# Kernel tuning notes

Measured on AMD Instinct MI355X. Metric: run time of the kernel, lower is better.

## Reference

```python
import jax, jax.numpy as jnp
import numpy as np

N, T, D, P, NB = 32768, 128, 32, 16, 15


def setup_inputs() -> dict:
    key = jax.random.key(0)
    ks = jax.random.split(key, 8)
    S = jax.random.normal(ks[0], (N, T, 1), dtype=jnp.float32)
    L_dyn = jax.random.normal(ks[1], (N, T, D), dtype=jnp.float32)
    C_static = jax.random.normal(ks[2], (N, P), dtype=jnp.float32)
    Y = jax.random.randint(ks[3], (N, T, 1), 0, 2).astype(jnp.float32)
    mask = jnp.ones((N, T), dtype=jnp.float32)
    return {
        "S": S, "L_dyn": L_dyn, "C_static": C_static, "Y": Y, "mask": mask,
        "psi": jnp.array([0.5], jnp.float32),
        "gamma_A": jnp.array([0.1], jnp.float32),
        "w_gamma_dyn": 0.05 * jax.random.normal(ks[4], (D,), dtype=jnp.float32),
        "w_gamma_static": 0.05 * jax.random.normal(ks[5], (P,), dtype=jnp.float32),
        "log_sigma_Z": jnp.array([-0.5], jnp.float32),
        "beta_0": jnp.array([-4.0], jnp.float32),
        "beta_Z": jnp.array([0.3], jnp.float32),
        "beta_bins": jnp.zeros((NB,), jnp.float32),
        "w_beta_dyn": 0.1 * jax.random.normal(ks[6], (D,), dtype=jnp.float32),
        "w_beta_static": 0.1 * jax.random.normal(ks[7], (P,), dtype=jnp.float32),
        "beta_time": jnp.array([0.03], jnp.float32),
    }


def reference(S, L_dyn, C_static, Y, mask, psi, gamma_A, w_gamma_dyn,
              w_gamma_static, log_sigma_Z, beta_0, beta_Z, beta_bins,
              w_beta_dyn, w_beta_static, beta_time):
    n, t_len = S.shape[0], S.shape[1]
    nb = beta_bins.shape[0]
    edges = jnp.linspace(-2.5, 2.5, nb + 1).astype(S.dtype)
    # torch.bucketize(s, edges[1:-1]) (right=False) == searchsorted side='left'
    idx = jnp.clip(jnp.searchsorted(edges[1:-1], S[..., 0], side='left'), 0, nb - 1)
    bin_eff = beta_bins[idx][..., None]            # (N,T,1) == (A_bin * beta_bins).sum(-1)
    sigma_sq = jnp.exp(log_sigma_Z)[0] ** 2        # sigma_Z^2
    gd = L_dyn @ w_gamma_dyn[:, None]              # (N,T,1) gamma_dyn(L)
    bd = L_dyn @ w_beta_dyn[:, None]               # (N,T,1) beta_dyn(L)
    gs = (C_static @ w_gamma_static)[:, None]      # (N,1) gamma_static(C)
    bs = (C_static @ w_beta_static)[:, None]       # (N,1) beta_static(C)
    tt = jnp.arange(t_len, dtype=S.dtype) / 30.0   # beta_time * (t/30)

    xs = (
        jnp.swapaxes(S, 0, 1),        # (T,N,1)
        jnp.swapaxes(gd, 0, 1),
        jnp.swapaxes(bd, 0, 1),
        jnp.swapaxes(bin_eff, 0, 1),
        jnp.swapaxes(Y, 0, 1),
        mask.T[:, :, None],           # (T,N,1)
        tt,
    )
    psi_s, gA, bZ, b0, bT = psi[0], gamma_A[0], beta_Z[0], beta_0[0], beta_time[0]

    def step(carry, x):
        Z_mean, Z_var, ll = carry
        A_t, gd_t, bd_t, be_t, Y_t, m_t, t_s = x
        # latent transition prior
        Z_pred_mean = psi_s * Z_mean + gA * A_t + gd_t + gs
        Z_pred_var = psi_s ** 2 * Z_var + sigma_sq
        # outcome probability
        logit = b0 + bZ * Z_pred_mean + be_t + bd_t + bs + bT * t_s
        prob = jax.nn.sigmoid(jnp.clip(logit, -20.0, 20.0))
        # approximate Kalman (Laplace) update from Y
        grad = (Y_t - prob) * bZ * m_t
        hess = bZ ** 2 * prob * (1.0 - prob) * m_t + 1e-6
        Z_post_var = 1.0 / (1.0 / (Z_pred_var + 1e-8) + hess)
        Z_post_mean = Z_pred_mean + Z_post_var * grad
        ll_t = ((Y_t * jnp.log(prob + 1e-10)
                 + (1.0 - Y_t) * jnp.log(1.0 - prob + 1e-10)) * m_t).sum()
        return (Z_post_mean, Z_post_var, ll + ll_t), (Z_post_mean, Z_post_var)

    init = (jnp.zeros((n, 1), S.dtype), jnp.ones((n, 1), S.dtype),
            jnp.zeros((), S.dtype))
    (_, _, ll), (Zf, Zv) = jax.lax.scan(step, init, xs)
    return jnp.swapaxes(Zf, 0, 1), jnp.swapaxes(Zv, 0, 1), ll
```

## Files before the change

kernel.cpp:

```cpp
#include <hip/hip_runtime.h>

#define T_LEN 128
#define NB_BINS 15

__global__ __launch_bounds__(256) void k_fused(
    const float4* __restrict__ S4,
    const float4* __restrict__ Y4,
    const float4* __restrict__ M4,
    const float4* __restrict__ C4,
    const float4* __restrict__ L4,
    const float4* __restrict__ wgd4,
    const float4* __restrict__ wbd4,
    const float4* __restrict__ wgs4,
    const float4* __restrict__ wbs4,
    const float*  __restrict__ p_psi,
    const float*  __restrict__ p_gA,
    const float*  __restrict__ p_lsz,
    const float*  __restrict__ p_b0,
    const float*  __restrict__ p_bZ,
    const float*  __restrict__ p_bbins,
    const float*  __restrict__ p_bT,
    float* __restrict__ zf,
    float* __restrict__ zv,
    float* __restrict__ ll_out)
{
    __shared__ float sbins[NB_BINS];
    if (threadIdx.x < NB_BINS) sbins[threadIdx.x] = p_bbins[threadIdx.x];
    __syncthreads();

    const int gtid = blockIdx.x * blockDim.x + threadIdx.x;
    const int n = gtid >> 2;
    const int s = gtid & 3;

    const float4 wga = wgd4[s * 2],     wgb = wgd4[s * 2 + 1];
    const float4 wba = wbd4[s * 2],     wbb = wbd4[s * 2 + 1];

    const float psi  = p_psi[0];
    const float gA   = p_gA[0];
    const float e    = expf(p_lsz[0]);
    const float sig2 = e * e;
    const float b0   = p_b0[0];
    const float bZ   = p_bZ[0];
    const float bT   = p_bT[0];
    const float psi2 = psi * psi;
    const float bZ2  = bZ * bZ;

    float gs, bs;
    {
        const float4 c  = C4[n * 4 + s];
        const float4 wg = wgs4[s];
        const float4 wb = wbs4[s];
        gs = c.x * wg.x + c.y * wg.y + c.z * wg.z + c.w * wg.w;
        bs = c.x * wb.x + c.y * wb.y + c.z * wb.z + c.w * wb.w;
        gs += __shfl_xor(gs, 1, 64); gs += __shfl_xor(gs, 2, 64);
        bs += __shfl_xor(bs, 1, 64); bs += __shfl_xor(bs, 2, 64);
    }

    const size_t lb  = (size_t)n * T_LEN * 8 + (size_t)s * 2;
    const int    sbi = n * (T_LEN / 4);

    float4 Lc0 = L4[lb + 0*8], Lc1 = L4[lb + 0*8 + 1];
    float4 Lc2 = L4[lb + 1*8], Lc3 = L4[lb + 1*8 + 1];
    float4 Lc4 = L4[lb + 2*8], Lc5 = L4[lb + 2*8 + 1];
    float4 Lc6 = L4[lb + 3*8], Lc7 = L4[lb + 3*8 + 1];
    float4 sc = S4[sbi], yc = Y4[sbi], mc = M4[sbi];

    float zm = 0.0f, zvv = 1.0f, ll = 0.0f;

#define STEP(J, LA, LB, SS, YY, MM, PMOUT, PVOUT) do {                        \
        const float s_v = (SS), y_v = (YY), m_v = (MM);                       \
        float g   = LA.x*wga.x + LA.y*wga.y + LA.z*wga.z + LA.w*wga.w         \
                  + LB.x*wgb.x + LB.y*wgb.y + LB.z*wgb.z + LB.w*wgb.w;        \
        float bdv = LA.x*wba.x + LA.y*wba.y + LA.z*wba.z + LA.w*wba.w         \
                  + LB.x*wbb.x + LB.y*wbb.y + LB.z*wbb.z + LB.w*wbb.w;        \
        g   += __shfl_xor(g,   1, 64); g   += __shfl_xor(g,   2, 64);         \
        bdv += __shfl_xor(bdv, 1, 64); bdv += __shfl_xor(bdv, 2, 64);         \
        int cnt = (int)fmaxf(0.0f, fminf(14.0f,                               \
                      ceilf(fmaf(s_v, 3.0f, 7.5f)) - 1.0f));                  \
        const float be    = sbins[cnt];                                       \
        const float zpm   = psi * zm + gA * s_v + g + gs;                     \
        const float zpv   = psi2 * zvv + sig2;                                \
        float logit = b0 + bZ * zpm + be + bdv + bs                           \
                    + bT * ((float)(4 * k + (J)) / 30.0f);                    \
        logit = fminf(fmaxf(logit, -20.0f), 20.0f);                           \
        const float prob  = 1.0f / (1.0f + expf(-logit));                     \
        const float grad  = (y_v - prob) * bZ * m_v;                          \
        const float hess  = bZ2 * prob * (1.0f - prob) * m_v + 1e-6f;         \
        const float pvv   = 1.0f / (1.0f / (zpv + 1e-8f) + hess);             \
        const float pmm   = zpm + pvv * grad;                                 \
        ll += (y_v * logf(prob + 1e-10f)                                      \
             + (1.0f - y_v) * logf(1.0f - prob + 1e-10f)) * m_v;              \
        zm = pmm; zvv = pvv; PMOUT = pmm; PVOUT = pvv;                        \
    } while (0)

    for (int k = 0; k < T_LEN / 4; ++k) {
        const int kn = (k + 1 < T_LEN / 4) ? (k + 1) : k;
        const size_t lbn = lb + (size_t)(4 * kn) * 8;
        float4 Ln0 = L4[lbn + 0*8], Ln1 = L4[lbn + 0*8 + 1];
        float4 Ln2 = L4[lbn + 1*8], Ln3 = L4[lbn + 1*8 + 1];
        float4 Ln4 = L4[lbn + 2*8], Ln5 = L4[lbn + 2*8 + 1];
        float4 Ln6 = L4[lbn + 3*8], Ln7 = L4[lbn + 3*8 + 1];
        float4 snn = S4[sbi + kn], ynn = Y4[sbi + kn], mnn = M4[sbi + kn];

        float pm0, pm1, pm2, pm3, pv0, pv1, pv2, pv3;
        STEP(0, Lc0, Lc1, sc.x, yc.x, mc.x, pm0, pv0);
        STEP(1, Lc2, Lc3, sc.y, yc.y, mc.y, pm1, pv1);
        STEP(2, Lc4, Lc5, sc.z, yc.z, mc.z, pm2, pv2);
        STEP(3, Lc6, Lc7, sc.w, yc.w, mc.w, pm3, pv3);

        const float pmsel = (s == 0) ? pm0 : (s == 1) ? pm1 : (s == 2) ? pm2 : pm3;
        const float pvsel = (s == 0) ? pv0 : (s == 1) ? pv1 : (s == 2) ? pv2 : pv3;
        const size_t oidx = (size_t)n * T_LEN + 4 * k + s;
        zf[oidx] = pmsel;
        zv[oidx] = pvsel;

        Lc0 = Ln0; Lc1 = Ln1; Lc2 = Ln2; Lc3 = Ln3;
        Lc4 = Ln4; Lc5 = Ln5; Lc6 = Ln6; Lc7 = Ln7;
        sc = snn; yc = ynn; mc = mnn;
    }
#undef STEP

    float lv = (s == 0) ? ll : 0.0f;
    #pragma unroll
    for (int off = 1; off < 64; off <<= 1) lv += __shfl_xor(lv, off, 64);
    if ((threadIdx.x & 63) == 0) atomicAdd(ll_out, lv);
}

extern "C" void kernel_launch(void* const* d_in, const int* in_sizes, int n_in,
                              void* d_out, int out_size, void* d_ws, size_t ws_size,
                              hipStream_t stream) {
    const float* S     = (const float*)d_in[0];
    const float* L     = (const float*)d_in[1];
    const float* C     = (const float*)d_in[2];
    const float* Y     = (const float*)d_in[3];
    const float* M     = (const float*)d_in[4];
    const float* psi   = (const float*)d_in[5];
    const float* gA    = (const float*)d_in[6];
    const float* wgd   = (const float*)d_in[7];
    const float* wgs   = (const float*)d_in[8];
    const float* lsz   = (const float*)d_in[9];
    const float* b0    = (const float*)d_in[10];
    const float* bZ    = (const float*)d_in[11];
    const float* bbins = (const float*)d_in[12];
    const float* wbd   = (const float*)d_in[13];
    const float* wbs   = (const float*)d_in[14];
    const float* bT    = (const float*)d_in[15];

    const int NT    = in_sizes[0];
    const int n_seq = NT / T_LEN;

    float* zf = (float*)d_out;
    float* zv = zf + NT;
    float* ll = zf + 2 * (size_t)NT;

    hipMemsetAsync((void*)ll, 0, sizeof(float), stream);

    const int threads = 256;
    const int blocks  = (n_seq * 4) / threads;
    k_fused<<<blocks, threads, 0, stream>>>(
        reinterpret_cast<const float4*>(S),
        reinterpret_cast<const float4*>(Y),
        reinterpret_cast<const float4*>(M),
        reinterpret_cast<const float4*>(C),
        reinterpret_cast<const float4*>(L),
        reinterpret_cast<const float4*>(wgd),
        reinterpret_cast<const float4*>(wbd),
        reinterpret_cast<const float4*>(wgs),
        reinterpret_cast<const float4*>(wbs),
        psi, gA, lsz, b0, bZ, bbins, bT,
        zf, zv, ll);
}
```

Before: 177.8 us.

## Distribute log-likelihood across lanes, interleave L loads, use fast intrinsics

Each of the four lanes sharing a sequence now computes the log-likelihood term only for its own timestep, instead of all four lanes redundantly evaluating two logs per step. The L_dyn loads are remapped so adjacent lanes read adjacent float4s, and the dyn-weight slices are permuted to match. Exact exp, log and divisions are replaced with __expf, __logf and hardware reciprocal intrinsics, and the 1/30 time scale is folded into one constant. This trims redundant transcendental work and improves load coalescing, at the cost of slightly lower numerical precision.

```diff
diff --git a/kernel.cpp b/kernel.cpp
--- a/kernel.cpp
+++ b/kernel.cpp
@@ -32,16 +32,16 @@
     const int n = gtid >> 2;
     const int s = gtid & 3;
 
-    const float4 wga = wgd4[s * 2],     wgb = wgd4[s * 2 + 1];
-    const float4 wba = wbd4[s * 2],     wbb = wbd4[s * 2 + 1];
+    const float4 wga = wgd4[s],     wgb = wgd4[s + 4];
+    const float4 wba = wbd4[s],     wbb = wbd4[s + 4];
 
     const float psi  = p_psi[0];
     const float gA   = p_gA[0];
-    const float e    = expf(p_lsz[0]);
+    const float e    = __expf(p_lsz[0]);
     const float sig2 = e * e;
     const float b0   = p_b0[0];
     const float bZ   = p_bZ[0];
-    const float bT   = p_bT[0];
+    const float bT30 = p_bT[0] * (1.0f / 30.0f);
     const float psi2 = psi * psi;
     const float bZ2  = bZ * bZ;
 
@@ -56,18 +56,18 @@
         bs += __shfl_xor(bs, 1, 64); bs += __shfl_xor(bs, 2, 64);
     }
 
-    const size_t lb  = (size_t)n * T_LEN * 8 + (size_t)s * 2;
+    const size_t lb  = (size_t)n * T_LEN * 8;
     const int    sbi = n * (T_LEN / 4);
 
-    float4 Lc0 = L4[lb + 0*8], Lc1 = L4[lb + 0*8 + 1];
-    float4 Lc2 = L4[lb + 1*8], Lc3 = L4[lb + 1*8 + 1];
-    float4 Lc4 = L4[lb + 2*8], Lc5 = L4[lb + 2*8 + 1];
-    float4 Lc6 = L4[lb + 3*8], Lc7 = L4[lb + 3*8 + 1];
+    float4 Lc0 = L4[lb + 0*8 + s], Lc1 = L4[lb + 0*8 + 4 + s];
+    float4 Lc2 = L4[lb + 1*8 + s], Lc3 = L4[lb + 1*8 + 4 + s];
+    float4 Lc4 = L4[lb + 2*8 + s], Lc5 = L4[lb + 2*8 + 4 + s];
+    float4 Lc6 = L4[lb + 3*8 + s], Lc7 = L4[lb + 3*8 + 4 + s];
     float4 sc = S4[sbi], yc = Y4[sbi], mc = M4[sbi];
 
     float zm = 0.0f, zvv = 1.0f, ll = 0.0f;
 
-#define STEP(J, LA, LB, SS, YY, MM, PMOUT, PVOUT) do {                        \
+#define STEP(J, LA, LB, SS, YY, MM, PMOUT, PVOUT, PROBOUT) do {               \
         const float s_v = (SS), y_v = (YY), m_v = (MM);                       \
         float g   = LA.x*wga.x + LA.y*wga.y + LA.z*wga.z + LA.w*wga.w         \
                   + LB.x*wgb.x + LB.y*wgb.y + LB.z*wgb.z + LB.w*wgb.w;        \
@@ -81,32 +81,31 @@
         const float zpm   = psi * zm + gA * s_v + g + gs;                     \
         const float zpv   = psi2 * zvv + sig2;                                \
         float logit = b0 + bZ * zpm + be + bdv + bs                           \
-                    + bT * ((float)(4 * k + (J)) / 30.0f);                    \
+                    + bT30 * (float)(4 * k + (J));                            \
         logit = fminf(fmaxf(logit, -20.0f), 20.0f);                           \
-        const float prob  = 1.0f / (1.0f + expf(-logit));                     \
+        const float prob  = __builtin_amdgcn_rcpf(1.0f + __expf(-logit));     \
         const float grad  = (y_v - prob) * bZ * m_v;                          \
         const float hess  = bZ2 * prob * (1.0f - prob) * m_v + 1e-6f;         \
-        const float pvv   = 1.0f / (1.0f / (zpv + 1e-8f) + hess);             \
+        const float pvv   = __builtin_amdgcn_rcpf(                            \
+                   __builtin_amdgcn_rcpf(zpv + 1e-8f) + hess);                \
         const float pmm   = zpm + pvv * grad;                                 \
-        ll += (y_v * logf(prob + 1e-10f)                                      \
-             + (1.0f - y_v) * logf(1.0f - prob + 1e-10f)) * m_v;              \
-        zm = pmm; zvv = pvv; PMOUT = pmm; PVOUT = pvv;                        \
+        zm = pmm; zvv = pvv; PMOUT = pmm; PVOUT = pvv; PROBOUT = prob;        \
     } while (0)
 
     for (int k = 0; k < T_LEN / 4; ++k) {
         const int kn = (k + 1 < T_LEN / 4) ? (k + 1) : k;
         const size_t lbn = lb + (size_t)(4 * kn) * 8;
-        float4 Ln0 = L4[lbn + 0*8], Ln1 = L4[lbn + 0*8 + 1];
-        float4 Ln2 = L4[lbn + 1*8], Ln3 = L4[lbn + 1*8 + 1];
-        float4 Ln4 = L4[lbn + 2*8], Ln5 = L4[lbn + 2*8 + 1];
-        float4 Ln6 = L4[lbn + 3*8], Ln7 = L4[lbn + 3*8 + 1];
+        float4 Ln0 = L4[lbn + 0*8 + s], Ln1 = L4[lbn + 0*8 + 4 + s];
+        float4 Ln2 = L4[lbn + 1*8 + s], Ln3 = L4[lbn + 1*8 + 4 + s];
+        float4 Ln4 = L4[lbn + 2*8 + s], Ln5 = L4[lbn + 2*8 + 4 + s];
+        float4 Ln6 = L4[lbn + 3*8 + s], Ln7 = L4[lbn + 3*8 + 4 + s];
         float4 snn = S4[sbi + kn], ynn = Y4[sbi + kn], mnn = M4[sbi + kn];
 
-        float pm0, pm1, pm2, pm3, pv0, pv1, pv2, pv3;
-        STEP(0, Lc0, Lc1, sc.x, yc.x, mc.x, pm0, pv0);
-        STEP(1, Lc2, Lc3, sc.y, yc.y, mc.y, pm1, pv1);
-        STEP(2, Lc4, Lc5, sc.z, yc.z, mc.z, pm2, pv2);
-        STEP(3, Lc6, Lc7, sc.w, yc.w, mc.w, pm3, pv3);
+        float pm0, pm1, pm2, pm3, pv0, pv1, pv2, pv3, pr0, pr1, pr2, pr3;
+        STEP(0, Lc0, Lc1, sc.x, yc.x, mc.x, pm0, pv0, pr0);
+        STEP(1, Lc2, Lc3, sc.y, yc.y, mc.y, pm1, pv1, pr1);
+        STEP(2, Lc4, Lc5, sc.z, yc.z, mc.z, pm2, pv2, pr2);
+        STEP(3, Lc6, Lc7, sc.w, yc.w, mc.w, pm3, pv3, pr3);
 
         const float pmsel = (s == 0) ? pm0 : (s == 1) ? pm1 : (s == 2) ? pm2 : pm3;
         const float pvsel = (s == 0) ? pv0 : (s == 1) ? pv1 : (s == 2) ? pv2 : pv3;
@@ -114,16 +113,23 @@
         zf[oidx] = pmsel;
         zv[oidx] = pvsel;
 
+        {
+            const float prs = (s == 0) ? pr0 : (s == 1) ? pr1 : (s == 2) ? pr2 : pr3;
+            const float ys  = (s == 0) ? yc.x : (s == 1) ? yc.y : (s == 2) ? yc.z : yc.w;
+            const float ms  = (s == 0) ? mc.x : (s == 1) ? mc.y : (s == 2) ? mc.z : mc.w;
+            ll += (ys * __logf(prs + 1e-10f)
+                 + (1.0f - ys) * __logf(1.0f - prs + 1e-10f)) * ms;
+        }
+
         Lc0 = Ln0; Lc1 = Ln1; Lc2 = Ln2; Lc3 = Ln3;
         Lc4 = Ln4; Lc5 = Ln5; Lc6 = Ln6; Lc7 = Ln7;
         sc = snn; yc = ynn; mc = mnn;
     }
 #undef STEP
 
-    float lv = (s == 0) ? ll : 0.0f;
     #pragma unroll
-    for (int off = 1; off < 64; off <<= 1) lv += __shfl_xor(lv, off, 64);
-    if ((threadIdx.x & 63) == 0) atomicAdd(ll_out, lv);
+    for (int off = 1; off < 64; off <<= 1) ll += __shfl_xor(ll, off, 64);
+    if ((threadIdx.x & 63) == 0) atomicAdd(ll_out, ll);
 }
 
 extern "C" void kernel_launch(void* const* d_in, const int* in_sizes, int n_in,
```

Measured after the change: 173.1 us. 2.6% less time.
